# Optimization experiments

Hardware: AMD Instinct MI355X
Metric: run time of the kernel (lower is better)

## Reference

```python
import jax, jax.numpy as jnp
import numpy as np

DIM = 1024
N_HEADS = 16
HEAD_DIM = DIM // N_HEADS


def setup_inputs() -> dict:
    key = jax.random.key(0)
    ks = jax.random.split(key, 7)
    B, S = 2, 2048
    scale = 0.02
    return {
        "q": jax.random.normal(ks[0], (B, S, DIM), dtype=jnp.float32),
        "k": jax.random.normal(ks[1], (B, S, DIM), dtype=jnp.float32),
        "v": jax.random.normal(ks[2], (B, S, DIM), dtype=jnp.float32),
        # torch nn.Linear weights are [out_features, in_features]; y = x @ W.T
        "wq": jax.random.normal(ks[3], (DIM, DIM), dtype=jnp.float32) * scale,
        "wk": jax.random.normal(ks[4], (DIM, DIM), dtype=jnp.float32) * scale,
        "wv": jax.random.normal(ks[5], (DIM, DIM), dtype=jnp.float32) * scale,
        "wo": jax.random.normal(ks[6], (DIM, DIM), dtype=jnp.float32) * scale,
    }


def reference(q, k, v, wq, wk, wv, wo):
    B, S, _ = q.shape
    H, D = N_HEADS, HEAD_DIM
    # projections (torch Linear: x @ W.T), reshape to [B, H, S, D]
    xq = (q @ wq.T).reshape(B, S, H, D).transpose(0, 2, 1, 3)
    xk = (k @ wk.T).reshape(B, S, H, D).transpose(0, 2, 1, 3)
    xv = (v @ wv.T).reshape(B, S, H, D).transpose(0, 2, 1, 3)
    # scaled dot-product attention with causal mask
    scores = jnp.einsum("bhqd,bhkd->bhqk", xq, xk) / jnp.sqrt(jnp.float32(D))
    causal = jnp.tril(jnp.ones((S, S), dtype=bool))
    scores = jnp.where(causal, scores, -jnp.inf)
    attn = jax.nn.softmax(scores.astype(jnp.float32), axis=-1).astype(xq.dtype)
    # dropout prob = 0.0 (eval-mode / deterministic reference)
    out = jnp.einsum("bhqk,bhkd->bhqd", attn, xv)
    out = out.transpose(0, 2, 1, 3).reshape(B, S, H * D)
    return out @ wo.T
```

## Files before the change

kernel.cpp:

```cpp
#include <hip/hip_runtime.h>
#include <hip/hip_bf16.h>
#include <stdint.h>


typedef short s16x8 __attribute__((ext_vector_type(8)));
typedef float f32x4 __attribute__((ext_vector_type(4)));

#define MFMA_BF16 __builtin_amdgcn_mfma_f32_16x16x32_bf16

static __device__ __forceinline__ unsigned short f2bf(float f) {
    union { float f; unsigned u; } x{f};
    unsigned r = x.u + 0x7fff + ((x.u >> 16) & 1);
    return (unsigned short)(r >> 16);
}
static __device__ __forceinline__ unsigned pk2h(float a, float b) {
    __hip_bfloat162 h = __float22bfloat162_rn(float2{a, b});
    return *(unsigned*)&h;
}

static __device__ __forceinline__ void ald16(unsigned short* lds, const unsigned short* g) {
    __builtin_amdgcn_global_load_lds(
        (const __attribute__((address_space(1))) unsigned int*)g,
        (__attribute__((address_space(3))) unsigned int*)lds, 16, 0, 0);
}

#define QSCL 0.18033688f

__global__ __launch_bounds__(256) void convert_all_kernel(
        const float* __restrict__ q, const float* __restrict__ k,
        const float* __restrict__ v,
        const float* __restrict__ wq, const float* __restrict__ wk,
        const float* __restrict__ wv, const float* __restrict__ wo,
        unsigned short* __restrict__ dst) {
    const size_t idx = ((size_t)blockIdx.x * 256 + threadIdx.x) * 8;
    const int region = (int)(idx >> 22);
    const float* src;
    size_t off;
    if (region == 0)      { src = q; off = idx; }
    else if (region == 1) { src = k; off = idx & 4194303; }
    else if (region == 2) { src = v; off = idx & 4194303; }
    else {
        const int wsel = (int)((idx >> 20) & 3);
        src = wsel == 0 ? wq : wsel == 1 ? wk : wsel == 2 ? wv : wo;
        off = idx & 1048575;
    }
    const float4* p = (const float4*)(src + off);
    float4 a = p[0], b = p[1];
    uint4 u;
    u.x = pk2h(a.x, a.y); u.y = pk2h(a.z, a.w);
    u.z = pk2h(b.x, b.y); u.w = pk2h(b.z, b.w);
    *(uint4*)(dst + idx) = u;
}

__global__ __launch_bounds__(256) void wconvert_kernel(
        const float* __restrict__ wq, const float* __restrict__ wk,
        const float* __restrict__ wv, const float* __restrict__ wo,
        unsigned short* __restrict__ Wb) {
    const size_t idx = ((size_t)blockIdx.x * 256 + threadIdx.x) * 8;
    const int region = (int)(idx >> 20);
    const size_t off = idx & 1048575;
    const float* src = region == 0 ? wq : region == 1 ? wk : region == 2 ? wv : wo;
    const float4* p = (const float4*)(src + off);
    float4 a = p[0], b = p[1];
    uint4 u;
    u.x = pk2h(a.x, a.y); u.y = pk2h(a.z, a.w);
    u.z = pk2h(b.x, b.y); u.w = pk2h(b.z, b.w);
    *(uint4*)(Wb + idx) = u;
}

__global__ __launch_bounds__(256) void proj3b_kernel(
        const unsigned short* __restrict__ Qb, const unsigned short* __restrict__ Kb,
        const unsigned short* __restrict__ Vb, const unsigned short* __restrict__ Wb,
        unsigned short* __restrict__ Xq, unsigned short* __restrict__ Xk,
        unsigned short* __restrict__ Xvt) {
    constexpr int Kd = 1024;
    __shared__ union {
        struct { unsigned short A[3][128 * 32]; unsigned short B[3][128 * 32]; } s;
        unsigned short T[4 * 64 * 68];
    } sm;

    const int z = blockIdx.z;
    const unsigned short* A  = z == 0 ? Qb : z == 1 ? Kb : Vb;
    const unsigned short* Bw = Wb + (size_t)z * 1048576;

    const int t = threadIdx.x;
    const int m0 = blockIdx.x * 128, n0 = blockIdx.y * 128;
    const int w = t >> 6, lane = t & 63, fr = lane & 15, g = lane >> 4;
    const int wm = (w >> 1) * 64, wn = (w & 1) * 64;
    const int brow = t >> 2;
    const int cB = (t & 3) ^ ((t >> 3) & 3);
    const int sB = g ^ ((fr >> 1) & 3);

    f32x4 acc[4][4] = {};

    auto STAGE = [&](int p, int kk) {
        ald16(sm.s.A[p] + (size_t)w * 512,        A  + (size_t)(m0 + brow) * Kd + kk + cB * 8);
        ald16(sm.s.A[p] + 2048 + (size_t)w * 512, A  + (size_t)(m0 + 64 + brow) * Kd + kk + cB * 8);
        ald16(sm.s.B[p] + (size_t)w * 512,        Bw + (size_t)(n0 + brow) * Kd + kk + cB * 8);
        ald16(sm.s.B[p] + 2048 + (size_t)w * 512, Bw + (size_t)(n0 + 64 + brow) * Kd + kk + cB * 8);
    };

    STAGE(0, 0);
    STAGE(1, 32);
    int bi = 0, nb = 2;

    for (int k0 = 0; k0 < Kd; k0 += 32) {
        if (k0 < Kd - 64) {
            STAGE(nb, k0 + 64);
            asm volatile("s_waitcnt vmcnt(8)" ::: "memory");
        } else if (k0 < Kd - 32) {
            asm volatile("s_waitcnt vmcnt(4)" ::: "memory");
        } else {
            asm volatile("s_waitcnt vmcnt(0)" ::: "memory");
        }
        __builtin_amdgcn_s_barrier();
        asm volatile("" ::: "memory");

        s16x8 af[4], bfv[4];
#pragma unroll
        for (int mi = 0; mi < 4; ++mi)
            af[mi] = *(const s16x8*)(sm.s.A[bi] + (wm + mi * 16 + fr) * 32 + sB * 8);
#pragma unroll
        for (int ni = 0; ni < 4; ++ni)
            bfv[ni] = *(const s16x8*)(sm.s.B[bi] + (wn + ni * 16 + fr) * 32 + sB * 8);
#pragma unroll
        for (int mi = 0; mi < 4; ++mi)
#pragma unroll
            for (int ni = 0; ni < 4; ++ni)
                acc[mi][ni] = MFMA_BF16(af[mi], bfv[ni], acc[mi][ni], 0, 0, 0);

        asm volatile("" ::: "memory");
        __builtin_amdgcn_s_barrier();
        bi = bi == 2 ? 0 : bi + 1;
        nb = nb == 2 ? 0 : nb + 1;
    }

    if (z != 2) {
        unsigned short* C = z ? Xk : Xq;
        const float osc = z == 0 ? QSCL : 1.0f;
#pragma unroll
        for (int mi = 0; mi < 4; ++mi)
#pragma unroll
            for (int ni = 0; ni < 4; ++ni)
#pragma unroll
                for (int reg = 0; reg < 4; ++reg)
                    C[(size_t)(m0 + wm + mi * 16 + g * 4 + reg) * 1024 +
                      n0 + wn + ni * 16 + fr] = f2bf(acc[mi][ni][reg] * osc);
    } else {
        unsigned short* T = sm.T + w * (64 * 68);
#pragma unroll
        for (int mi = 0; mi < 4; ++mi)
#pragma unroll
            for (int ni = 0; ni < 4; ++ni) {
                uint2 u;
                u.x = pk2h(acc[mi][ni][0], acc[mi][ni][1]);
                u.y = pk2h(acc[mi][ni][2], acc[mi][ni][3]);
                *(uint2*)(T + (ni * 16 + fr) * 68 + mi * 16 + g * 4) = u;
            }
        __asm__ __volatile__("" ::: "memory");
#pragma unroll
        for (int pass = 0; pass < 8; ++pass) {
            const int row = pass * 8 + (lane >> 3);
            const int chk = lane & 7;
            uint4 d = *(const uint4*)(T + row * 68 + chk * 8);
            *(uint4*)(Xvt + (size_t)(n0 + wn + row) * 4096 + m0 + wm + chk * 8) = d;
        }
    }
}

__global__ __launch_bounds__(256) void proj3_kernel(
        const float* __restrict__ q, const float* __restrict__ k, const float* __restrict__ v,
        const unsigned short* __restrict__ Wb,
        unsigned short* __restrict__ Xq, unsigned short* __restrict__ Xk,
        unsigned short* __restrict__ Xvt) {
    constexpr int Kd = 1024;
    __shared__ unsigned short lsA[128 * 40];
    __shared__ unsigned short lsB[128 * 32];
    __shared__ unsigned short Tls[4 * 64 * 68];

    const int z = blockIdx.z;
    const float* A = z == 0 ? q : z == 1 ? k : v;
    const unsigned short* Bw = Wb + (size_t)z * 1048576;

    const int t = threadIdx.x;
    const int m0 = blockIdx.x * 128, n0 = blockIdx.y * 128;
    const int w = t >> 6, lane = t & 63, fr = lane & 15, g = lane >> 4, fq = g * 8;
    const int wm = (w >> 1) * 64, wn = (w & 1) * 64;
    const int ar = t >> 1, ac = (t & 1) * 16;
    const int brow = t >> 2;
    const int cB = (t & 3) ^ ((t >> 3) & 3);
    const int sB = g ^ ((fr >> 1) & 3);

    f32x4 acc[4][4] = {};

    for (int k0 = 0; k0 < Kd; k0 += 32) {
        ald16(lsB + (size_t)w * 512,        Bw + (size_t)(n0 + brow) * Kd + k0 + cB * 8);
        ald16(lsB + 2048 + (size_t)w * 512, Bw + (size_t)(n0 + 64 + brow) * Kd + k0 + cB * 8);
        {
            const float4* pa = (const float4*)(A + (size_t)(m0 + ar) * Kd + k0 + ac);
            float4 a0 = pa[0], a1 = pa[1], a2 = pa[2], a3 = pa[3];
            uint4 u0, u1;
            u0.x = pk2h(a0.x, a0.y); u0.y = pk2h(a0.z, a0.w);
            u0.z = pk2h(a1.x, a1.y); u0.w = pk2h(a1.z, a1.w);
            u1.x = pk2h(a2.x, a2.y); u1.y = pk2h(a2.z, a2.w);
            u1.z = pk2h(a3.x, a3.y); u1.w = pk2h(a3.z, a3.w);
            *(uint4*)(lsA + ar * 40 + ac)     = u0;
            *(uint4*)(lsA + ar * 40 + ac + 8) = u1;
        }
        __syncthreads();

        s16x8 af[4], bfv[4];
#pragma unroll
        for (int mi = 0; mi < 4; ++mi)
            af[mi] = *(const s16x8*)(lsA + (wm + mi * 16 + fr) * 40 + fq);
#pragma unroll
        for (int ni = 0; ni < 4; ++ni)
            bfv[ni] = *(const s16x8*)(lsB + (wn + ni * 16 + fr) * 32 + sB * 8);
#pragma unroll
        for (int mi = 0; mi < 4; ++mi)
#pragma unroll
            for (int ni = 0; ni < 4; ++ni)
                acc[mi][ni] = MFMA_BF16(af[mi], bfv[ni], acc[mi][ni], 0, 0, 0);
        __syncthreads();
    }

    if (z != 2) {
        unsigned short* C = z ? Xk : Xq;
        const float osc = z == 0 ? QSCL : 1.0f;
#pragma unroll
        for (int mi = 0; mi < 4; ++mi)
#pragma unroll
            for (int ni = 0; ni < 4; ++ni)
#pragma unroll
                for (int reg = 0; reg < 4; ++reg)
                    C[(size_t)(m0 + wm + mi * 16 + g * 4 + reg) * 1024 +
                      n0 + wn + ni * 16 + fr] = f2bf(acc[mi][ni][reg] * osc);
    } else {
        unsigned short* T = Tls + w * (64 * 68);
#pragma unroll
        for (int mi = 0; mi < 4; ++mi)
#pragma unroll
            for (int ni = 0; ni < 4; ++ni) {
                uint2 u;
                u.x = pk2h(acc[mi][ni][0], acc[mi][ni][1]);
                u.y = pk2h(acc[mi][ni][2], acc[mi][ni][3]);
                *(uint2*)(T + (ni * 16 + fr) * 68 + mi * 16 + g * 4) = u;
            }
        __asm__ __volatile__("" ::: "memory");
#pragma unroll
        for (int pass = 0; pass < 8; ++pass) {
            const int row = pass * 8 + (lane >> 3);
            const int chk = lane & 7;
            uint4 d = *(const uint4*)(T + row * 68 + chk * 8);
            *(uint4*)(Xvt + (size_t)(n0 + wn + row) * 4096 + m0 + wm + chk * 8) = d;
        }
    }
}

static __device__ __forceinline__ void slab_tail(
        const f32x4 sf[4], int kt, int qt, int qrow, float& l_part,
        f32x4* oacc, unsigned short* Pw, const s16x8 vf[4][2], int fr, int g) {
    float e[4][4];
    const bool diag = (kt == qt);
#pragma unroll
    for (int m16 = 0; m16 < 4; ++m16)
#pragma unroll
        for (int r = 0; r < 4; ++r) {
            float x = sf[m16][r];
            if (diag) {
                const int keyg = kt * 64 + m16 * 16 + g * 4 + r;
                x = (keyg <= qrow) ? x : -1e30f;
            }
            const float ee = __builtin_amdgcn_exp2f(x);
            e[m16][r] = ee;
            l_part += ee;
        }
#pragma unroll
    for (int m16 = 0; m16 < 4; ++m16) {
        uint2 u;
        u.x = pk2h(e[m16][0], e[m16][1]);
        u.y = pk2h(e[m16][2], e[m16][3]);
        const int ch = 2 * m16 + (g >> 1);
        *(uint2*)(Pw + fr * 64 + ((ch ^ (fr & 7)) * 8) + (g & 1) * 4) = u;
    }
    __asm__ __volatile__("" ::: "memory");
    s16x8 pf0 = *(const s16x8*)(Pw + fr * 64 + ((g ^ (fr & 7)) * 8));
    s16x8 pf1 = *(const s16x8*)(Pw + fr * 64 + (((4 + g) ^ (fr & 7)) * 8));
    __builtin_amdgcn_s_setprio(1);
#pragma unroll
    for (int m16 = 0; m16 < 4; ++m16) {
        oacc[m16] = MFMA_BF16(vf[m16][0], pf0, oacc[m16], 0, 0, 0);
        oacc[m16] = MFMA_BF16(vf[m16][1], pf1, oacc[m16], 0, 0, 0);
    }
    __builtin_amdgcn_s_setprio(0);
    __asm__ __volatile__("" ::: "memory");
}

__global__ __launch_bounds__(256, 2) void flash_attn_kernel(
        const unsigned short* __restrict__ Xq, const unsigned short* __restrict__ Xk,
        const unsigned short* __restrict__ Xvt, unsigned short* __restrict__ Oa) {
    __shared__ unsigned short Kls[2][64 * 64];
    __shared__ unsigned short Vls[2][64 * 64];
    __shared__ unsigned short Pls[4][16 * 64];

    const int t = threadIdx.x;
    const int bh = blockIdx.x;
    const int j = blockIdx.y;
    const int b = bh >> 4, h = bh & 15;
    const size_t rbase = (size_t)b * 2048;
    const int cbase = h * 64;

    const int w = t >> 6, lane = t & 63, fr = lane & 15, g = lane >> 4, fq = g * 8;
    const int qtH = 31 - j, qtL = j;
    const int qrowH = qtH * 64 + w * 16 + fr;
    const int qrowL = qtL * 64 + w * 16 + fr;

    const unsigned short* qpH = Xq + (rbase + qrowH) * 1024 + cbase;
    s16x8 qfH0 = *(const s16x8*)(qpH + fq);
    s16x8 qfH1 = *(const s16x8*)(qpH + 32 + fq);
    const unsigned short* qpL = Xq + (rbase + qrowL) * 1024 + cbase;
    s16x8 qfL0 = *(const s16x8*)(qpL + fq);
    s16x8 qfL1 = *(const s16x8*)(qpL + 32 + fq);

    float lH = 0.f, lL = 0.f;
    f32x4 oH[4] = {}, oL[4] = {};

    const int r0 = w * 16 + (lane >> 3), r1 = r0 + 8;
    const int s8 = lane & 7;
    const int c0 = s8 ^ (r0 & 7), c1 = s8 ^ (r1 & 7);
    const unsigned short* kbase = Xk + rbase * 1024 + cbase;
    const size_t vrow0 = (size_t)(cbase + r0) * 4096 + rbase + c0 * 8;
    const size_t vrow1 = (size_t)(cbase + r1) * 4096 + rbase + c1 * 8;

    uint4 kA = *(const uint4*)(kbase + (size_t)r0 * 1024 + c0 * 8);
    uint4 kB = *(const uint4*)(kbase + (size_t)r1 * 1024 + c1 * 8);
    uint4 vA = *(const uint4*)(Xvt + vrow0);
    uint4 vB = *(const uint4*)(Xvt + vrow1);

    *(uint4*)(Kls[0] + (w * 16) * 64 + lane * 8)     = kA;
    *(uint4*)(Kls[0] + (w * 16 + 8) * 64 + lane * 8) = kB;
    *(uint4*)(Vls[0] + (w * 16) * 64 + lane * 8)     = vA;
    *(uint4*)(Vls[0] + (w * 16 + 8) * 64 + lane * 8) = vB;
    __syncthreads();

    for (int kt = 0; kt <= qtH; ++kt) {
        const int cur = kt & 1;

        if (kt < qtH) {
            const unsigned short* ks = kbase + (size_t)(kt + 1) * 65536;
            kA = *(const uint4*)(ks + (size_t)r0 * 1024 + c0 * 8);
            kB = *(const uint4*)(ks + (size_t)r1 * 1024 + c1 * 8);
            vA = *(const uint4*)(Xvt + vrow0 + (size_t)(kt + 1) * 64);
            vB = *(const uint4*)(Xvt + vrow1 + (size_t)(kt + 1) * 64);
        }

        const bool doL = (kt <= qtL);

        s16x8 kf[4][2], vf[4][2];
#pragma unroll
        for (int m16 = 0; m16 < 4; ++m16) {
            const int rr = m16 * 16 + fr;
            kf[m16][0] = *(const s16x8*)(Kls[cur] + rr * 64 + ((g ^ (fr & 7)) * 8));
            kf[m16][1] = *(const s16x8*)(Kls[cur] + rr * 64 + (((4 + g) ^ (fr & 7)) * 8));
            vf[m16][0] = *(const s16x8*)(Vls[cur] + rr * 64 + ((g ^ (fr & 7)) * 8));
            vf[m16][1] = *(const s16x8*)(Vls[cur] + rr * 64 + (((4 + g) ^ (fr & 7)) * 8));
        }

        f32x4 sH[4], sL[4];
        __builtin_amdgcn_s_setprio(1);
#pragma unroll
        for (int m16 = 0; m16 < 4; ++m16) {
            f32x4 zz = {};
            zz = MFMA_BF16(kf[m16][0], qfH0, zz, 0, 0, 0);
            sH[m16] = MFMA_BF16(kf[m16][1], qfH1, zz, 0, 0, 0);
        }
        if (doL) {
#pragma unroll
            for (int m16 = 0; m16 < 4; ++m16) {
                f32x4 zz = {};
                zz = MFMA_BF16(kf[m16][0], qfL0, zz, 0, 0, 0);
                sL[m16] = MFMA_BF16(kf[m16][1], qfL1, zz, 0, 0, 0);
            }
        }
        __builtin_amdgcn_s_setprio(0);

        slab_tail(sH, kt, qtH, qrowH, lH, oH, &Pls[w][0], vf, fr, g);
        if (doL)
            slab_tail(sL, kt, qtL, qrowL, lL, oL, &Pls[w][0], vf, fr, g);

        if (kt < qtH) {
            const int nxt = cur ^ 1;
            *(uint4*)(Kls[nxt] + (w * 16) * 64 + lane * 8)     = kA;
            *(uint4*)(Kls[nxt] + (w * 16 + 8) * 64 + lane * 8) = kB;
            *(uint4*)(Vls[nxt] + (w * 16) * 64 + lane * 8)     = vA;
            *(uint4*)(Vls[nxt] + (w * 16 + 8) * 64 + lane * 8) = vB;
            __syncthreads();
        }
    }

    lH += __shfl_xor(lH, 16, 64);
    lH += __shfl_xor(lH, 32, 64);
    lL += __shfl_xor(lL, 16, 64);
    lL += __shfl_xor(lL, 32, 64);
    const float invH = 1.0f / lH, invL = 1.0f / lL;
#pragma unroll
    for (int m16 = 0; m16 < 4; ++m16) {
        uint2 u;
        u.x = pk2h(oH[m16][0] * invH, oH[m16][1] * invH);
        u.y = pk2h(oH[m16][2] * invH, oH[m16][3] * invH);
        *(uint2*)(Oa + (rbase + qrowH) * 1024 + cbase + m16 * 16 + g * 4) = u;
        uint2 u2;
        u2.x = pk2h(oL[m16][0] * invL, oL[m16][1] * invL);
        u2.y = pk2h(oL[m16][2] * invL, oL[m16][3] * invL);
        *(uint2*)(Oa + (rbase + qrowL) * 1024 + cbase + m16 * 16 + g * 4) = u2;
    }
}

__global__ __launch_bounds__(256) void outproj_kernel(
        const unsigned short* __restrict__ Oa, const unsigned short* __restrict__ Wo,
        float* __restrict__ out) {
    constexpr int Kd = 1024;
    __shared__ unsigned short lsA[2][2][64 * 32];
    __shared__ unsigned short lsB[2][2][128 * 32];

    const int t = threadIdx.x;
    const int m0 = blockIdx.x * 64, n0 = blockIdx.y * 128;
    const int w = t >> 6, lane = t & 63, fr = lane & 15, g = lane >> 4;
    const int wm = (w >> 1) * 32, wn = (w & 1) * 64;
    const int brow = t >> 2;
    const int cB = (t & 3) ^ ((t >> 3) & 3);
    const int sB = g ^ ((fr >> 1) & 3);

    f32x4 acc[2][4] = {};

    auto STAGE = [&](int p, int kk) {
#pragma unroll
        for (int sub = 0; sub < 2; ++sub) {
            const int ks = kk + sub * 32;
            ald16(lsA[p][sub] + (size_t)w * 512,        Oa + (size_t)(m0 + brow) * Kd + ks + cB * 8);
            ald16(lsB[p][sub] + (size_t)w * 512,        Wo + (size_t)(n0 + brow) * Kd + ks + cB * 8);
            ald16(lsB[p][sub] + 2048 + (size_t)w * 512, Wo + (size_t)(n0 + 64 + brow) * Kd + ks + cB * 8);
        }
    };

    STAGE(0, 0);
    int buf = 0;

    for (int it = 0; it < 16; ++it) {
        if (it < 15) {
            STAGE(buf ^ 1, (it + 1) * 64);
            asm volatile("s_waitcnt vmcnt(6)" ::: "memory");
        } else {
            asm volatile("s_waitcnt vmcnt(0)" ::: "memory");
        }
        __builtin_amdgcn_s_barrier();
        asm volatile("" ::: "memory");

#pragma unroll
        for (int sub = 0; sub < 2; ++sub) {
            s16x8 af[2], bfv[4];
#pragma unroll
            for (int mi = 0; mi < 2; ++mi)
                af[mi] = *(const s16x8*)(lsA[buf][sub] + (wm + mi * 16 + fr) * 32 + sB * 8);
#pragma unroll
            for (int ni = 0; ni < 4; ++ni)
                bfv[ni] = *(const s16x8*)(lsB[buf][sub] + (wn + ni * 16 + fr) * 32 + sB * 8);
#pragma unroll
            for (int mi = 0; mi < 2; ++mi)
#pragma unroll
                for (int ni = 0; ni < 4; ++ni)
                    acc[mi][ni] = MFMA_BF16(af[mi], bfv[ni], acc[mi][ni], 0, 0, 0);
        }

        asm volatile("" ::: "memory");
        __builtin_amdgcn_s_barrier();
        buf ^= 1;
    }

#pragma unroll
    for (int mi = 0; mi < 2; ++mi)
#pragma unroll
        for (int ni = 0; ni < 4; ++ni)
#pragma unroll
            for (int reg = 0; reg < 4; ++reg)
                out[(size_t)(m0 + wm + mi * 16 + g * 4 + reg) * 1024 +
                    n0 + wn + ni * 16 + fr] = acc[mi][ni][reg];
}

extern "C" void kernel_launch(void* const* d_in, const int* in_sizes, int n_in,
                              void* d_out, int out_size, void* d_ws, size_t ws_size,
                              hipStream_t stream) {
    const float* q  = (const float*)d_in[0];
    const float* k  = (const float*)d_in[1];
    const float* v  = (const float*)d_in[2];
    const float* wq = (const float*)d_in[3];
    const float* wk = (const float*)d_in[4];
    const float* wv = (const float*)d_in[5];
    const float* wo = (const float*)d_in[6];
    float* out = (float*)d_out;

    if (ws_size >= (size_t)64 * 1024 * 1024) {
        unsigned short* base = (unsigned short*)d_ws;
        unsigned short* Qb  = base;
        unsigned short* Kb  = base + 4194304;
        unsigned short* Vb  = base + 8388608;
        unsigned short* Wb  = base + 12582912;
        unsigned short* Xq  = base + 16777216;
        unsigned short* Xk  = base + 20971520;
        unsigned short* Xvt = base + 25165824;
        unsigned short* Oa  = base + 29360128;

        convert_all_kernel<<<8192, 256, 0, stream>>>(q, k, v, wq, wk, wv, wo, base);
        proj3b_kernel<<<dim3(32, 8, 3), 256, 0, stream>>>(Qb, Kb, Vb, Wb, Xq, Xk, Xvt);
        flash_attn_kernel<<<dim3(32, 16), 256, 0, stream>>>(Xq, Xk, Xvt, Oa);
        outproj_kernel<<<dim3(64, 8), 256, 0, stream>>>(Oa, Wb + 3145728, out);
    } else {
        unsigned short* Wb  = (unsigned short*)d_ws;
        unsigned short* Xq  = Wb  + 4194304;
        unsigned short* Xk  = Xq  + 4194304;
        unsigned short* Xvt = Xk  + 4194304;
        unsigned short* Oa  = Xvt + 4194304;

        wconvert_kernel<<<2048, 256, 0, stream>>>(wq, wk, wv, wo, Wb);
        proj3_kernel<<<dim3(32, 8, 3), 256, 0, stream>>>(q, k, v, Wb, Xq, Xk, Xvt);
        flash_attn_kernel<<<dim3(32, 16), 256, 0, stream>>>(Xq, Xk, Xvt, Oa);
        outproj_kernel<<<dim3(64, 8), 256, 0, stream>>>(Oa, Wb + 3145728, out);
    }
}
```

Baseline: 194.7 us.

## Fuse fp32 activation conversion into pipelined projection GEMM, drop separate convert pass

Removes the separate full-activation bf16 conversion kernel and the bf16-input projection kernel. The fp32 projection kernel is rewritten with a double-buffered A tile and a triple-buffered B tile, so the next A tile is loaded from global into registers while the MFMAs run, then converted and written to LDS. This removes the extra round trip of writing and re-reading bf16 activations. In exchange, each GEMM block now reads fp32 activations (twice the bytes) and does the conversion inline, which could add register pressure.

```diff
diff --git a/kernel.cpp b/kernel.cpp
--- a/kernel.cpp
+++ b/kernel.cpp
@@ -25,32 +25,6 @@
 }
 
 #define QSCL 0.18033688f
-
-__global__ __launch_bounds__(256) void convert_all_kernel(
-        const float* __restrict__ q, const float* __restrict__ k,
-        const float* __restrict__ v,
-        const float* __restrict__ wq, const float* __restrict__ wk,
-        const float* __restrict__ wv, const float* __restrict__ wo,
-        unsigned short* __restrict__ dst) {
-    const size_t idx = ((size_t)blockIdx.x * 256 + threadIdx.x) * 8;
-    const int region = (int)(idx >> 22);
-    const float* src;
-    size_t off;
-    if (region == 0)      { src = q; off = idx; }
-    else if (region == 1) { src = k; off = idx & 4194303; }
-    else if (region == 2) { src = v; off = idx & 4194303; }
-    else {
-        const int wsel = (int)((idx >> 20) & 3);
-        src = wsel == 0 ? wq : wsel == 1 ? wk : wsel == 2 ? wv : wo;
-        off = idx & 1048575;
-    }
-    const float4* p = (const float4*)(src + off);
-    float4 a = p[0], b = p[1];
-    uint4 u;
-    u.x = pk2h(a.x, a.y); u.y = pk2h(a.z, a.w);
-    u.z = pk2h(b.x, b.y); u.w = pk2h(b.z, b.w);
-    *(uint4*)(dst + idx) = u;
-}
 
 __global__ __launch_bounds__(256) void wconvert_kernel(
         const float* __restrict__ wq, const float* __restrict__ wk,
@@ -68,115 +42,16 @@
     *(uint4*)(Wb + idx) = u;
 }
 
-__global__ __launch_bounds__(256) void proj3b_kernel(
-        const unsigned short* __restrict__ Qb, const unsigned short* __restrict__ Kb,
-        const unsigned short* __restrict__ Vb, const unsigned short* __restrict__ Wb,
-        unsigned short* __restrict__ Xq, unsigned short* __restrict__ Xk,
-        unsigned short* __restrict__ Xvt) {
-    constexpr int Kd = 1024;
-    __shared__ union {
-        struct { unsigned short A[3][128 * 32]; unsigned short B[3][128 * 32]; } s;
-        unsigned short T[4 * 64 * 68];
-    } sm;
-
-    const int z = blockIdx.z;
-    const unsigned short* A  = z == 0 ? Qb : z == 1 ? Kb : Vb;
-    const unsigned short* Bw = Wb + (size_t)z * 1048576;
-
-    const int t = threadIdx.x;
-    const int m0 = blockIdx.x * 128, n0 = blockIdx.y * 128;
-    const int w = t >> 6, lane = t & 63, fr = lane & 15, g = lane >> 4;
-    const int wm = (w >> 1) * 64, wn = (w & 1) * 64;
-    const int brow = t >> 2;
-    const int cB = (t & 3) ^ ((t >> 3) & 3);
-    const int sB = g ^ ((fr >> 1) & 3);
-
-    f32x4 acc[4][4] = {};
-
-    auto STAGE = [&](int p, int kk) {
-        ald16(sm.s.A[p] + (size_t)w * 512,        A  + (size_t)(m0 + brow) * Kd + kk + cB * 8);
-        ald16(sm.s.A[p] + 2048 + (size_t)w * 512, A  + (size_t)(m0 + 64 + brow) * Kd + kk + cB * 8);
-        ald16(sm.s.B[p] + (size_t)w * 512,        Bw + (size_t)(n0 + brow) * Kd + kk + cB * 8);
-        ald16(sm.s.B[p] + 2048 + (size_t)w * 512, Bw + (size_t)(n0 + 64 + brow) * Kd + kk + cB * 8);
-    };
-
-    STAGE(0, 0);
-    STAGE(1, 32);
-    int bi = 0, nb = 2;
-
-    for (int k0 = 0; k0 < Kd; k0 += 32) {
-        if (k0 < Kd - 64) {
-            STAGE(nb, k0 + 64);
-            asm volatile("s_waitcnt vmcnt(8)" ::: "memory");
-        } else if (k0 < Kd - 32) {
-            asm volatile("s_waitcnt vmcnt(4)" ::: "memory");
-        } else {
-            asm volatile("s_waitcnt vmcnt(0)" ::: "memory");
-        }
-        __builtin_amdgcn_s_barrier();
-        asm volatile("" ::: "memory");
-
-        s16x8 af[4], bfv[4];
-#pragma unroll
-        for (int mi = 0; mi < 4; ++mi)
-            af[mi] = *(const s16x8*)(sm.s.A[bi] + (wm + mi * 16 + fr) * 32 + sB * 8);
-#pragma unroll
-        for (int ni = 0; ni < 4; ++ni)
-            bfv[ni] = *(const s16x8*)(sm.s.B[bi] + (wn + ni * 16 + fr) * 32 + sB * 8);
-#pragma unroll
-        for (int mi = 0; mi < 4; ++mi)
-#pragma unroll
-            for (int ni = 0; ni < 4; ++ni)
-                acc[mi][ni] = MFMA_BF16(af[mi], bfv[ni], acc[mi][ni], 0, 0, 0);
-
-        asm volatile("" ::: "memory");
-        __builtin_amdgcn_s_barrier();
-        bi = bi == 2 ? 0 : bi + 1;
-        nb = nb == 2 ? 0 : nb + 1;
-    }
-
-    if (z != 2) {
-        unsigned short* C = z ? Xk : Xq;
-        const float osc = z == 0 ? QSCL : 1.0f;
-#pragma unroll
-        for (int mi = 0; mi < 4; ++mi)
-#pragma unroll
-            for (int ni = 0; ni < 4; ++ni)
-#pragma unroll
-                for (int reg = 0; reg < 4; ++reg)
-                    C[(size_t)(m0 + wm + mi * 16 + g * 4 + reg) * 1024 +
-                      n0 + wn + ni * 16 + fr] = f2bf(acc[mi][ni][reg] * osc);
-    } else {
-        unsigned short* T = sm.T + w * (64 * 68);
-#pragma unroll
-        for (int mi = 0; mi < 4; ++mi)
-#pragma unroll
-            for (int ni = 0; ni < 4; ++ni) {
-                uint2 u;
-                u.x = pk2h(acc[mi][ni][0], acc[mi][ni][1]);
-                u.y = pk2h(acc[mi][ni][2], acc[mi][ni][3]);
-                *(uint2*)(T + (ni * 16 + fr) * 68 + mi * 16 + g * 4) = u;
-            }
-        __asm__ __volatile__("" ::: "memory");
-#pragma unroll
-        for (int pass = 0; pass < 8; ++pass) {
-            const int row = pass * 8 + (lane >> 3);
-            const int chk = lane & 7;
-            uint4 d = *(const uint4*)(T + row * 68 + chk * 8);
-            *(uint4*)(Xvt + (size_t)(n0 + wn + row) * 4096 + m0 + wm + chk * 8) = d;
-        }
-    }
-}
-
-__global__ __launch_bounds__(256) void proj3_kernel(
+__global__ __launch_bounds__(256) void projf_kernel(
         const float* __restrict__ q, const float* __restrict__ k, const float* __restrict__ v,
         const unsigned short* __restrict__ Wb,
         unsigned short* __restrict__ Xq, unsigned short* __restrict__ Xk,
         unsigned short* __restrict__ Xvt) {
     constexpr int Kd = 1024;
-    __shared__ unsigned short lsA[128 * 40];
-    __shared__ unsigned short lsB[128 * 32];
-    __shared__ unsigned short Tls[4 * 64 * 68];
+    __shared__ union {
+        struct { unsigned short A[2][128 * 40]; unsigned short B[3][128 * 32]; } s;
+        unsigned short T[4 * 64 * 68];
+    } sm;
 
     const int z = blockIdx.z;
     const float* A = z == 0 ? q : z == 1 ? k : v;
@@ -191,37 +66,65 @@
     const int cB = (t & 3) ^ ((t >> 3) & 3);
     const int sB = g ^ ((fr >> 1) & 3);
 
+    const float* arow = A + (size_t)(m0 + ar) * Kd + ac;
+
     f32x4 acc[4][4] = {};
 
-    for (int k0 = 0; k0 < Kd; k0 += 32) {
-        ald16(lsB + (size_t)w * 512,        Bw + (size_t)(n0 + brow) * Kd + k0 + cB * 8);
-        ald16(lsB + 2048 + (size_t)w * 512, Bw + (size_t)(n0 + 64 + brow) * Kd + k0 + cB * 8);
-        {
-            const float4* pa = (const float4*)(A + (size_t)(m0 + ar) * Kd + k0 + ac);
-            float4 a0 = pa[0], a1 = pa[1], a2 = pa[2], a3 = pa[3];
-            uint4 u0, u1;
-            u0.x = pk2h(a0.x, a0.y); u0.y = pk2h(a0.z, a0.w);
-            u0.z = pk2h(a1.x, a1.y); u0.w = pk2h(a1.z, a1.w);
-            u1.x = pk2h(a2.x, a2.y); u1.y = pk2h(a2.z, a2.w);
-            u1.z = pk2h(a3.x, a3.y); u1.w = pk2h(a3.z, a3.w);
-            *(uint4*)(lsA + ar * 40 + ac)     = u0;
-            *(uint4*)(lsA + ar * 40 + ac + 8) = u1;
-        }
-        __syncthreads();
+    auto STAGE_B = [&](int p, int kk) {
+        ald16(sm.s.B[p] + (size_t)w * 512,        Bw + (size_t)(n0 + brow) * Kd + kk + cB * 8);
+        ald16(sm.s.B[p] + 2048 + (size_t)w * 512, Bw + (size_t)(n0 + 64 + brow) * Kd + kk + cB * 8);
+    };
+    auto CONV_WRITE_A = [&](int p, float4 a0, float4 a1, float4 a2, float4 a3) {
+        uint4 u0, u1;
+        u0.x = pk2h(a0.x, a0.y); u0.y = pk2h(a0.z, a0.w);
+        u0.z = pk2h(a1.x, a1.y); u0.w = pk2h(a1.z, a1.w);
+        u1.x = pk2h(a2.x, a2.y); u1.y = pk2h(a2.z, a2.w);
+        u1.z = pk2h(a3.x, a3.y); u1.w = pk2h(a3.z, a3.w);
+        *(uint4*)(sm.s.A[p] + ar * 40 + ac)     = u0;
+        *(uint4*)(sm.s.A[p] + ar * 40 + ac + 8) = u1;
+    };
+
+    STAGE_B(0, 0);
+    float4 a0, a1, a2, a3;
+    {
+        const float4* pa = (const float4*)(arow);
+        a0 = pa[0]; a1 = pa[1]; a2 = pa[2]; a3 = pa[3];
+    }
+    CONV_WRITE_A(0, a0, a1, a2, a3);
+    STAGE_B(1, 32);
+    asm volatile("s_waitcnt lgkmcnt(0)" ::: "memory");
+    __builtin_amdgcn_s_barrier();
+    asm volatile("" ::: "memory");
+
+    for (int it = 0; it < 32; ++it) {
+        const int k0 = it * 32;
+        const int ab = it & 1, bb = it % 3;
+
+        if (it < 31) {
+            const float4* pa = (const float4*)(arow + k0 + 32);
+            a0 = pa[0]; a1 = pa[1]; a2 = pa[2]; a3 = pa[3];
+        }
 
         s16x8 af[4], bfv[4];
 #pragma unroll
         for (int mi = 0; mi < 4; ++mi)
-            af[mi] = *(const s16x8*)(lsA + (wm + mi * 16 + fr) * 40 + fq);
+            af[mi] = *(const s16x8*)(sm.s.A[ab] + (wm + mi * 16 + fr) * 40 + fq);
 #pragma unroll
         for (int ni = 0; ni < 4; ++ni)
-            bfv[ni] = *(const s16x8*)(lsB + (wn + ni * 16 + fr) * 32 + sB * 8);
+            bfv[ni] = *(const s16x8*)(sm.s.B[bb] + (wn + ni * 16 + fr) * 32 + sB * 8);
 #pragma unroll
         for (int mi = 0; mi < 4; ++mi)
 #pragma unroll
             for (int ni = 0; ni < 4; ++ni)
                 acc[mi][ni] = MFMA_BF16(af[mi], bfv[ni], acc[mi][ni], 0, 0, 0);
-        __syncthreads();
+
+        if (it < 31) {
+            CONV_WRITE_A(ab ^ 1, a0, a1, a2, a3);
+            if (it < 30) STAGE_B((it + 2) % 3, k0 + 64);
+            asm volatile("s_waitcnt lgkmcnt(0)" ::: "memory");
+            __builtin_amdgcn_s_barrier();
+            asm volatile("" ::: "memory");
+        }
     }
 
     if (z != 2) {
@@ -236,7 +139,8 @@
                     C[(size_t)(m0 + wm + mi * 16 + g * 4 + reg) * 1024 +
                       n0 + wn + ni * 16 + fr] = f2bf(acc[mi][ni][reg] * osc);
     } else {
-        unsigned short* T = Tls + w * (64 * 68);
+        __syncthreads();
+        unsigned short* T = sm.T + w * (64 * 68);
 #pragma unroll
         for (int mi = 0; mi < 4; ++mi)
 #pragma unroll
@@ -499,31 +403,14 @@
     const float* wo = (const float*)d_in[6];
     float* out = (float*)d_out;
 
-    if (ws_size >= (size_t)64 * 1024 * 1024) {
-        unsigned short* base = (unsigned short*)d_ws;
-        unsigned short* Qb  = base;
-        unsigned short* Kb  = base + 4194304;
-        unsigned short* Vb  = base + 8388608;
-        unsigned short* Wb  = base + 12582912;
-        unsigned short* Xq  = base + 16777216;
-        unsigned short* Xk  = base + 20971520;
-        unsigned short* Xvt = base + 25165824;
-        unsigned short* Oa  = base + 29360128;
-
-        convert_all_kernel<<<8192, 256, 0, stream>>>(q, k, v, wq, wk, wv, wo, base);
-        proj3b_kernel<<<dim3(32, 8, 3), 256, 0, stream>>>(Qb, Kb, Vb, Wb, Xq, Xk, Xvt);
-        flash_attn_kernel<<<dim3(32, 16), 256, 0, stream>>>(Xq, Xk, Xvt, Oa);
-        outproj_kernel<<<dim3(64, 8), 256, 0, stream>>>(Oa, Wb + 3145728, out);
-    } else {
-        unsigned short* Wb  = (unsigned short*)d_ws;
-        unsigned short* Xq  = Wb  + 4194304;
-        unsigned short* Xk  = Xq  + 4194304;
-        unsigned short* Xvt = Xk  + 4194304;
-        unsigned short* Oa  = Xvt + 4194304;
-
-        wconvert_kernel<<<2048, 256, 0, stream>>>(wq, wk, wv, wo, Wb);
-        proj3_kernel<<<dim3(32, 8, 3), 256, 0, stream>>>(q, k, v, Wb, Xq, Xk, Xvt);
-        flash_attn_kernel<<<dim3(32, 16), 256, 0, stream>>>(Xq, Xk, Xvt, Oa);
-        outproj_kernel<<<dim3(64, 8), 256, 0, stream>>>(Oa, Wb + 3145728, out);
-    }
-}
+    unsigned short* Wb  = (unsigned short*)d_ws;
+    unsigned short* Xq  = Wb  + 4194304;
+    unsigned short* Xk  = Xq  + 4194304;
+    unsigned short* Xvt = Xk  + 4194304;
+    unsigned short* Oa  = Xvt + 4194304;
+
+    wconvert_kernel<<<2048, 256, 0, stream>>>(wq, wk, wv, wo, Wb);
+    projf_kernel<<<dim3(32, 8, 3), 256, 0, stream>>>(q, k, v, Wb, Xq, Xk, Xvt);
+    flash_attn_kernel<<<dim3(32, 16), 256, 0, stream>>>(Xq, Xk, Xvt, Oa);
+    outproj_kernel<<<dim3(64, 8), 256, 0, stream>>>(Oa, Wb + 3145728, out);
+}
```

After: 203.1 us. 4.3% more time.
